# Kernel optimization log

Hardware: AMD Instinct MI355X
Metric: run time of the kernel (lower is better)

## Reference

```python
import jax, jax.numpy as jnp
import numpy as np

B, T, C = 4, 2048, 1024
NH = 16
HD = C // NH  # 64


def setup_inputs() -> dict:
    key = jax.random.key(0)
    k1, k2, k3 = jax.random.split(key, 3)
    x = jax.random.normal(k1, (B, T, C), dtype=jnp.float32)
    # causal mask buffer, 1 = keep, 0 = mask out
    mask = jnp.tril(jnp.ones((T, T), dtype=jnp.int32))[None, None, :, :]
    # learned params (Linear with bias=False): torch stores weight as [out, in],
    # y = x @ W.T ; we store transposed for direct matmul
    w_qkv = jax.random.normal(k2, (C, 3 * C), dtype=jnp.float32) / np.sqrt(C)
    w_proj = jax.random.normal(k3, (C, C), dtype=jnp.float32) / np.sqrt(C)
    return {"x": x, "mask": mask, "w_qkv": w_qkv, "w_proj": w_proj}


def reference(x, mask, w_qkv, w_proj):
    b, t, c = x.shape
    qkv = x @ w_qkv  # [b, t, 3c]
    q, k, v = jnp.split(qkv, 3, axis=-1)
    # [b, nh, t, hd]
    q = q.reshape(b, t, NH, HD).transpose(0, 2, 1, 3)
    k = k.reshape(b, t, NH, HD).transpose(0, 2, 1, 3)
    v = v.reshape(b, t, NH, HD).transpose(0, 2, 1, 3)
    att = jnp.einsum("bhqd,bhkd->bhqk", q, k) * (1.0 / np.sqrt(HD))
    att = jnp.where(mask == 0, -jnp.inf, att)
    att = jax.nn.softmax(att, axis=-1)
    y = jnp.einsum("bhqk,bhkd->bhqd", att, v)
    y = y.transpose(0, 2, 1, 3).reshape(b, t, c)
    return y @ w_proj
```

## Files before the change

kernel.cpp:

```cpp
#include <hip/hip_runtime.h>
#include <hip/hip_bf16.h>

typedef _Float16 f16;
typedef __attribute__((ext_vector_type(2))) __fp16 fp16x2;
typedef __attribute__((ext_vector_type(4))) _Float16 f16x4;
typedef __attribute__((ext_vector_type(8))) _Float16 f16x8;
typedef __attribute__((ext_vector_type(4))) float f32x4;

#define MFMA16(a, b, c) __builtin_amdgcn_mfma_f32_16x16x16f16((a), (b), (c), 0, 0, 0)
#define MFMA32(a, b, c) __builtin_amdgcn_mfma_f32_16x16x32_f16((a), (b), (c), 0, 0, 0)
#define EXP2(x) __builtin_amdgcn_exp2f(x)
#define GLOAD_LDS16(g, l)                                                        \
  __builtin_amdgcn_global_load_lds((const __attribute__((address_space(1))) void*)(g), \
                                   (__attribute__((address_space(3))) void*)(l), 16, 0, 0)
typedef const __attribute__((address_space(3))) char* lds_cp;
#define TR16(dst, addr, imm) \
  asm volatile("ds_read_b64_tr_b16 %0, %1 offset:" imm : "=v"(dst) : "v"(addr))

__global__ __launch_bounds__(256) void prep_kernel(
    const float* __restrict__ x, f16* __restrict__ x16,
    const float* __restrict__ wq, f16* __restrict__ wqT,
    const float* __restrict__ wp, f16* __restrict__ wpT) {
  const int blk = blockIdx.x;
  const int tid = threadIdx.x;
  if (blk < 8192) {
    int i = blk * 256 + tid;
    const float4 v = reinterpret_cast<const float4*>(x)[i];
    f16x4 h;
    h[0] = (f16)v.x; h[1] = (f16)v.y; h[2] = (f16)v.z; h[3] = (f16)v.w;
    reinterpret_cast<f16x4*>(x16)[i] = h;
    return;
  }
  const float* src;
  f16* dst;
  int R, Cc, bx, by;
  if (blk < 11264) {
    int j = blk - 8192;
    bx = j % 96; by = j / 96;
    src = wq; dst = wqT; R = 1024; Cc = 3072;
  } else {
    int j = blk - 11264;
    bx = j & 31; by = j >> 5;
    src = wp; dst = wpT; R = 1024; Cc = 1024;
  }
  __shared__ float t[32][33];
  int tx0 = bx * 32, ty0 = by * 32;
  int c = tid & 31;
  int r0 = tid >> 5;
#pragma unroll
  for (int i = 0; i < 4; i++) {
    int r = r0 + 8 * i;
    t[r][c] = src[(size_t)(ty0 + r) * Cc + tx0 + c];
  }
  __syncthreads();
#pragma unroll
  for (int i = 0; i < 4; i++) {
    int a = r0 + 8 * i;
    dst[(size_t)(tx0 + a) * R + ty0 + c] = (f16)t[c][a];
  }
}

template <bool OUT_F32>
__global__ __launch_bounds__(512, 2) void gemm_deep_kernel(
    const f16* __restrict__ A, const f16* __restrict__ Bt, void* __restrict__ Cout,
    int M, int N, int K) {
  __shared__ __align__(16) char smem[147456];
  const int tid = threadIdx.x;
  const int lane = tid & 63, wid = tid >> 6;
  const int wm = wid >> 2, wn = wid & 3;
  const int lo = lane & 15, hi = lane >> 4;

  const int ntn = N >> 7;
  const int nwg = (M >> 8) * ntn;
  const int wg = (blockIdx.x & 7) * (nwg >> 3) + (blockIdx.x >> 3);
  const int tm0 = (wg / ntn) << 8;
  const int tn0 = (wg % ntn) << 7;

  const int prow = tid >> 3;
  const int u8 = (tid & 7) ^ (prow & 7);
  const f16* asrc[4];
  const f16* bsrc[2];
#pragma unroll
  for (int c = 0; c < 4; c++) asrc[c] = A + (size_t)(tm0 + c * 64 + prow) * K + u8 * 8;
#pragma unroll
  for (int c = 0; c < 2; c++) bsrc[c] = Bt + (size_t)(tn0 + c * 64 + prow) * K + u8 * 8;

  const int swz = lo & 7;
  const int s0 = (hi ^ swz) << 4, s1 = ((4 + hi) ^ swz) << 4;
  const int abase0 = wm * 16384 + lo * 128 + s0;
  const int abase1 = wm * 16384 + lo * 128 + s1;
  int boff0[2], boff1[2];
#pragma unroll
  for (int ni = 0; ni < 2; ni++) {
    int g = 2 * wn + ni;
    int base = 32768 + (g >> 2) * 8192 + ((g & 3) * 16 + lo) * 128;
    boff0[ni] = base + s0;
    boff1[ni] = base + s1;
  }

  f32x4 acc[8][2] = {};

  auto stage = [&](int kt, char* buf) {
    const int ke = kt << 6;
#pragma unroll
    for (int c = 0; c < 4; c++)
      GLOAD_LDS16(asrc[c] + ke, buf + c * 8192 + tid * 16);
#pragma unroll
    for (int c = 0; c < 2; c++)
      GLOAD_LDS16(bsrc[c] + ke, buf + 32768 + c * 8192 + tid * 16);
  };

  const int NT = K >> 6;
  stage(0, smem);
  stage(1, smem + 49152);

  int bufi = 0;
  for (int t = 0; t < NT; t++) {
    char* db = smem + bufi * 49152;
    if (t + 1 < NT) {
      asm volatile("s_waitcnt vmcnt(6)" ::: "memory");
    } else {
      asm volatile("s_waitcnt vmcnt(0)" ::: "memory");
    }
    __builtin_amdgcn_s_barrier();
    if (t + 2 < NT) {
      int nb = bufi + 2;
      if (nb >= 3) nb -= 3;
      stage(t + 2, smem + nb * 49152);
    }
    __builtin_amdgcn_sched_barrier(0);

    f16x8 a[8][2], b[2][2];
#pragma unroll
    for (int mi = 0; mi < 8; mi++) {
      int off = (mi >> 2) * 8192 + (mi & 3) * 2048;
      a[mi][0] = *(const f16x8*)(db + abase0 + off);
      a[mi][1] = *(const f16x8*)(db + abase1 + off);
    }
#pragma unroll
    for (int ni = 0; ni < 2; ni++) {
      b[ni][0] = *(const f16x8*)(db + boff0[ni]);
      b[ni][1] = *(const f16x8*)(db + boff1[ni]);
    }
    __builtin_amdgcn_s_setprio(1);
#pragma unroll
    for (int mi = 0; mi < 8; mi++)
#pragma unroll
      for (int ni = 0; ni < 2; ni++) {
        acc[mi][ni] = MFMA32(a[mi][0], b[ni][0], acc[mi][ni]);
        acc[mi][ni] = MFMA32(a[mi][1], b[ni][1], acc[mi][ni]);
      }
    __builtin_amdgcn_s_setprio(0);

    bufi = (bufi == 2) ? 0 : bufi + 1;
  }

#pragma unroll
  for (int mi = 0; mi < 8; mi++)
#pragma unroll
    for (int ni = 0; ni < 2; ni++)
#pragma unroll
      for (int r = 0; r < 4; r++) {
        int row = tm0 + wm * 128 + mi * 16 + 4 * hi + r;
        int col = tn0 + wn * 32 + ni * 16 + lo;
        float v = acc[mi][ni][r];
        if (OUT_F32)
          ((float*)Cout)[(size_t)row * N + col] = v;
        else
          ((f16*)Cout)[(size_t)row * N + col] = (f16)v;
      }
}

__global__ __launch_bounds__(512, 2) void attn_kernel(
    const f16* __restrict__ qkv, f16* __restrict__ y) {
  constexpr int T = 2048, NHD = 3072, LDO = 72;
  const int bh = blockIdx.x;
  const int b = bh >> 4, h = bh & 15;
  const int pr = blockIdx.y;
  const int tid = threadIdx.x;
  const int lane = tid & 63, w = tid >> 6;
  const int lo = lane & 15, hi = lane >> 4;

  const size_t base = (size_t)b * T * NHD + (size_t)h * 64;
  const f16* Qp = qkv + base;
  const f16* Kp = qkv + base + 1024;
  const f16* Vp = qkv + base + 2048;

  __shared__ __align__(16) char smem[32768];
  f16 (*Ol)[LDO] = (f16(*)[LDO])smem;

  const int mytile = (w < 4) ? pr : (31 - pr);
  const int qb = mytile * 64 + (w & 3) * 16;

  const float scf = 0.125f * 1.44269504089f;
  f16x8 qf[2];
  {
    const f16* qrow = Qp + (size_t)(qb + lo) * NHD;
#pragma unroll
    for (int ks = 0; ks < 2; ks++) {
      f16x8 v = *(const f16x8*)&qrow[ks * 32 + 8 * hi];
#pragma unroll
      for (int j = 0; j < 8; j++) v[j] = (f16)((float)v[j] * scf);
      qf[ks] = v;
    }
  }

  f32x4 oacc[4] = {};
  f32x4 lacc = {};
  const f16x4 ones4 = {(f16)1.f, (f16)1.f, (f16)1.f, (f16)1.f};

  const int kr = tid >> 3;
  const int kslot = (tid & 7) ^ (kr & 7);
  const int vkey = 4 * ((tid & 127) >> 3) + ((tid >> 1) & 3);
  const int vcol = (tid >> 7) * 16 + (tid & 1) * 8;

  const int kfo0 = lo * 64 + ((hi ^ (lo & 7)) * 8);
  const int kfo1 = lo * 64 + (((4 + hi) ^ (lo & 7)) * 8);

  auto stage = [&](int kv, int c) {
    char* kb = smem + c * 8192;
    char* vb = smem + 16384 + c * 8192;
    GLOAD_LDS16(&Kp[(size_t)(kv + kr) * NHD + kslot * 8], kb + tid * 16);
    GLOAD_LDS16(&Vp[(size_t)(kv + vkey) * NHD + vcol], vb + tid * 16);
  };

  const int nt = 32 - pr;
  stage(0, 0);
  asm volatile("s_waitcnt vmcnt(0)" ::: "memory");
  __builtin_amdgcn_s_barrier();

  for (int t = 0; t < nt; t++) {
    const int cur = t & 1;
    const int kv0 = t * 64;
    if (t + 1 < nt) stage(kv0 + 64, cur ^ 1);

    if (kv0 <= qb + 15) {
      const f16* Kl = (const f16*)(smem + cur * 8192);
      f16x8 kf0[4], kf1[4];
#pragma unroll
      for (int ct = 0; ct < 4; ct++) {
        kf0[ct] = *(const f16x8*)&Kl[ct * 1024 + kfo0];
        kf1[ct] = *(const f16x8*)&Kl[ct * 1024 + kfo1];
      }
      f32x4 s_[4] = {};
      __builtin_amdgcn_s_setprio(1);
#pragma unroll
      for (int ct = 0; ct < 4; ct++) s_[ct] = MFMA32(kf0[ct], qf[0], s_[ct]);
#pragma unroll
      for (int ct = 0; ct < 4; ct++) s_[ct] = MFMA32(kf1[ct], qf[1], s_[ct]);
      __builtin_amdgcn_s_setprio(0);

      lds_cp vtrb = (lds_cp)(smem + 16384 + cur * 8192) + lane * 8;
      f16x4 v[4][4];
#pragma unroll
      for (int ct = 0; ct < 4; ct++) {
        lds_cp bct = vtrb + ct * 2048;
        TR16(v[ct][0], bct, "0");
        TR16(v[ct][1], bct, "512");
        TR16(v[ct][2], bct, "1024");
        TR16(v[ct][3], bct, "1536");
      }

      if (kv0 + 63 > qb) {
        const int q = qb + lo;
#pragma unroll
        for (int ct = 0; ct < 4; ct++)
#pragma unroll
          for (int r = 0; r < 4; r++)
            if (kv0 + ct * 16 + 4 * hi + r > q) s_[ct][r] = -3.0e38f;
      }
      f16x4 pb[4];
#pragma unroll
      for (int ct = 0; ct < 4; ct++) {
        float p0 = EXP2(s_[ct][0]), p1 = EXP2(s_[ct][1]);
        float p2 = EXP2(s_[ct][2]), p3 = EXP2(s_[ct][3]);
        union { f16x4 vv; fp16x2 hh[2]; } u;
        u.hh[0] = __builtin_amdgcn_cvt_pkrtz(p0, p1);
        u.hh[1] = __builtin_amdgcn_cvt_pkrtz(p2, p3);
        pb[ct] = u.vv;
      }
      __builtin_amdgcn_s_setprio(1);
#pragma unroll
      for (int kk = 0; kk < 4; kk++) lacc = MFMA16(ones4, pb[kk], lacc);
      __builtin_amdgcn_s_setprio(0);

      asm volatile("s_waitcnt lgkmcnt(0)" ::: "memory");
      __builtin_amdgcn_sched_barrier(0);
      __builtin_amdgcn_s_setprio(1);
#pragma unroll
      for (int ct = 0; ct < 4; ct++) {
        oacc[ct] = MFMA16(v[ct][0], pb[0], oacc[ct]);
        oacc[ct] = MFMA16(v[ct][1], pb[1], oacc[ct]);
        oacc[ct] = MFMA16(v[ct][2], pb[2], oacc[ct]);
        oacc[ct] = MFMA16(v[ct][3], pb[3], oacc[ct]);
      }
      __builtin_amdgcn_s_setprio(0);
    }

    asm volatile("s_waitcnt vmcnt(0)" ::: "memory");
    __builtin_amdgcn_s_barrier();
  }

  const float inv = 1.f / lacc[0];
#pragma unroll
  for (int ct = 0; ct < 4; ct++) {
    f16x4 o4;
#pragma unroll
    for (int r = 0; r < 4; r++) o4[r] = (f16)(oacc[ct][r] * inv);
    *(f16x4*)&Ol[w * 16 + lo][ct * 16 + 4 * hi] = o4;
  }
  __syncthreads();
#pragma unroll
  for (int i = 0; i < 2; i++) {
    int idx = tid + 512 * i;
    int qq = idx >> 3, ch = idx & 7;
    int row = ((qq < 64) ? pr : (31 - pr)) * 64 + (qq & 63);
    *(f16x8*)&y[((size_t)b * T + row) * 1024 + (size_t)h * 64 + ch * 8] =
        *(const f16x8*)&Ol[qq][ch * 8];
  }
}

extern "C" void kernel_launch(void* const* d_in, const int* in_sizes, int n_in,
                              void* d_out, int out_size, void* d_ws, size_t ws_size,
                              hipStream_t stream) {
  const float* x = (const float*)d_in[0];
  const float* w_qkv = (const float*)d_in[2];
  const float* w_proj = (const float*)d_in[3];

  constexpr int B = 4, T = 2048, C = 1024, NH = 16;
  constexpr int M = B * T;
  constexpr int N1 = 3 * C;

  char* ws = (char*)d_ws;
  f16* x16 = (f16*)ws;    ws += (size_t)M * C * 2;
  f16* wqkvT = (f16*)ws;  ws += (size_t)N1 * C * 2;
  f16* wprojT = (f16*)ws; ws += (size_t)C * C * 2;
  f16* qkvb = (f16*)ws;   ws += (size_t)M * N1 * 2;
  f16* y16 = (f16*)ws;

  prep_kernel<<<12288, 256, 0, stream>>>(x, x16, w_qkv, wqkvT, w_proj, wprojT);
  gemm_deep_kernel<false><<<(M / 256) * (N1 / 128), 512, 0, stream>>>(x16, wqkvT, qkvb, M, N1, C);
  attn_kernel<<<dim3(B * NH, 16), 512, 0, stream>>>(qkvb, y16);
  gemm_deep_kernel<true><<<(M / 256) * (C / 128), 512, 0, stream>>>(y16, wprojT, (float*)d_out, M, C, C);
}
```

Baseline: 165.0 us.

## Add dedicated QKV GEMM kernel with 256x384 tiles sized to one wave

Replaces the generic QKV projection GEMM with a specialized kernel that uses 256x384 output tiles. This gives 256 workgroups, which fills the GPU in a single wave instead of leaving a partial tail wave. Each warp computes an 8x6 MFMA block per k-step, which raises reuse of each loaded fragment. The kernel uses a two-stage LDS double buffer of 160KB, so the pipeline is shallower than before and occupancy is limited to one block per CU. Its epilogue writes individual f16 elements, which may be less efficient than vectorized stores.

```diff
diff --git a/kernel.cpp b/kernel.cpp
--- a/kernel.cpp
+++ b/kernel.cpp
@@ -60,6 +60,83 @@
   }
 }
 
+__global__ __launch_bounds__(512, 2) void gemm_qkv_kernel(
+    const f16* __restrict__ A, const f16* __restrict__ Bt, f16* __restrict__ C,
+    int M, int N, int K) {
+  __shared__ __align__(16) char smem[163840];
+  const int tid = threadIdx.x;
+  const int lane = tid & 63, wid = tid >> 6;
+  const int wm = wid >> 2, wn = wid & 3;
+  const int lo = lane & 15, hi = lane >> 4;
+
+  const int ntn = N / 384;
+  const int nwg = (M >> 8) * ntn;
+  const int wg = (blockIdx.x & 7) * (nwg >> 3) + (blockIdx.x >> 3);
+  const int tm0 = (wg / ntn) << 8;
+  const int tn0 = (wg % ntn) * 384;
+
+  const int prow = tid >> 3;
+  const int u8 = (tid & 7) ^ (prow & 7);
+  const f16* a0 = A + (size_t)(tm0 + prow) * K + u8 * 8;
+  const f16* b0 = Bt + (size_t)(tn0 + prow) * K + u8 * 8;
+
+  const int swz = lo & 7;
+  const int as0 = (hi ^ swz) << 4, as1 = ((4 + hi) ^ swz) << 4;
+  const int abase = (wm * 128 + lo) * 128;
+  const int bbase = 32768 + (wn * 96 + lo) * 128;
+
+  f32x4 acc[8][6] = {};
+
+  auto stage = [&](int ke, char* buf) {
+#pragma unroll
+    for (int c = 0; c < 4; c++)
+      GLOAD_LDS16(a0 + (size_t)c * 64 * K + ke, buf + c * 8192 + tid * 16);
+#pragma unroll
+    for (int c = 0; c < 6; c++)
+      GLOAD_LDS16(b0 + (size_t)c * 64 * K + ke, buf + 32768 + c * 8192 + tid * 16);
+  };
+
+  const int NT = K >> 6;
+  stage(0, smem);
+
+  for (int t = 0; t < NT; t++) {
+    char* db = smem + (t & 1) * 81920;
+    asm volatile("s_waitcnt vmcnt(0)" ::: "memory");
+    __builtin_amdgcn_s_barrier();
+    if (t + 1 < NT) stage((t + 1) << 6, smem + ((t + 1) & 1) * 81920);
+    __builtin_amdgcn_sched_barrier(0);
+
+#pragma unroll
+    for (int ks = 0; ks < 2; ks++) {
+      const int so = ks ? as1 : as0;
+      f16x8 b[6];
+#pragma unroll
+      for (int ni = 0; ni < 6; ni++)
+        b[ni] = *(const f16x8*)(db + bbase + ni * 2048 + so);
+      __builtin_amdgcn_s_setprio(1);
+#pragma unroll
+      for (int mi = 0; mi < 8; mi++) {
+        f16x8 a = *(const f16x8*)(db + abase + mi * 2048 + so);
+#pragma unroll
+        for (int ni = 0; ni < 6; ni++)
+          acc[mi][ni] = MFMA32(a, b[ni], acc[mi][ni]);
+      }
+      __builtin_amdgcn_s_setprio(0);
+    }
+  }
+
+#pragma unroll
+  for (int mi = 0; mi < 8; mi++)
+#pragma unroll
+    for (int ni = 0; ni < 6; ni++)
+#pragma unroll
+      for (int r = 0; r < 4; r++) {
+        int row = tm0 + wm * 128 + mi * 16 + 4 * hi + r;
+        int col = tn0 + wn * 96 + ni * 16 + lo;
+        C[(size_t)row * N + col] = (f16)acc[mi][ni][r];
+      }
+}
+
 template <bool OUT_F32>
 __global__ __launch_bounds__(512, 2) void gemm_deep_kernel(
     const f16* __restrict__ A, const f16* __restrict__ Bt, void* __restrict__ Cout,
@@ -339,7 +416,7 @@
   f16* y16 = (f16*)ws;
 
   prep_kernel<<<12288, 256, 0, stream>>>(x, x16, w_qkv, wqkvT, w_proj, wprojT);
-  gemm_deep_kernel<false><<<(M / 256) * (N1 / 128), 512, 0, stream>>>(x16, wqkvT, qkvb, M, N1, C);
+  gemm_qkv_kernel<<<(M / 256) * (N1 / 384), 512, 0, stream>>>(x16, wqkvT, qkvb, M, N1, C);
   attn_kernel<<<dim3(B * NH, 16), 512, 0, stream>>>(qkvb, y16);
   gemm_deep_kernel<true><<<(M / 256) * (C / 128), 512, 0, stream>>>(y16, wprojT, (float*)d_out, M, C, C);
 }
```

New measurement: 144.0 us (median of 2 runs). 1.15x faster.
